# Kernel tuning notes

Hardware: AMD Instinct MI355X
Metric: run time of the kernel (lower is better)

Reference implementation:

```python
import jax, jax.numpy as jnp
import numpy as np

EPS = 1e-5  # matches torch default epsilon


def setup_inputs() -> dict:
    key = jax.random.key(0)
    ks = jax.random.split(key, 7)
    B, S, H = 32, 8192, 128
    return {
        "time_to_maturity": jax.random.uniform(ks[0], (B, S), jnp.float32),
        "log_moneyness": jax.random.normal(ks[1], (B, S), jnp.float32),
        "target_variance": jax.random.uniform(ks[2], (B, S), jnp.float32),
        "W1": jax.random.normal(ks[3], (2, H), jnp.float32) * 0.5,
        "b1": jax.random.normal(ks[4], (H,), jnp.float32) * 0.1,
        "W2": jax.random.normal(ks[5], (H,), jnp.float32) * 0.5,
        "b2": jax.random.normal(ks[6], (1,), jnp.float32) * 0.1,
    }


def reference(time_to_maturity, log_moneyness, target_variance, W1, b1, W2, b2):
    # Upstream surface model: elementwise (t, x) -> total implied variance w > 0.
    def w_fn(t, x):
        h = jnp.tanh(t * W1[0] + x * W1[1] + b1)  # [H]
        return jax.nn.softplus(jnp.dot(h, W2) + b2[0])  # scalar

    w_t_fn = jax.grad(w_fn, argnums=0)
    w_x_fn = jax.grad(w_fn, argnums=1)
    w_xx_fn = jax.grad(w_x_fn, argnums=1)

    tf = time_to_maturity.reshape(-1)   # [N] flattened query points
    xf = log_moneyness.reshape(-1)
    tgt = target_variance.reshape(-1)
    N = tf.shape[0]

    # Diagonal Jacobian entries: replaces the O(N^2) unit-vector autograd loop.
    w = jax.vmap(w_fn)(tf, xf)
    w_t = jax.vmap(w_t_fn)(tf, xf)
    w_x = jax.vmap(w_x_fn)(tf, xf)
    w_xx = jax.vmap(w_xx_fn)(tf, xf)

    percentage_error = (w - tgt) / (tgt + EPS)
    mspe = jnp.sum(percentage_error ** 2)

    calendar = jnp.sum(jnp.maximum(-w_t, 0.0) ** 2)

    # Durrleman butterfly condition g(x)
    g = (1.0 - xf * w_x / (2.0 * w)) ** 2 - (w_x / 4.0) * (1.0 / w + 0.25) + w_xx / 2.0
    butterfly = jnp.sum(jnp.maximum(-g, 0.0) ** 2)

    return jnp.stack([mspe, calendar, butterfly]) / N
```

## Files before the change

kernel.cpp:

```cpp
#include <hip/hip_runtime.h>
#include <cmath>

#define HDIM 128
constexpr float EPSF = 1e-5f;
constexpr float K2L  = 2.8853900817779268f;
constexpr float INVK = 0.34657359027997264f;
constexpr float L2E  = 1.4426950408889634f;
constexpr float LN2  = 0.6931471805599453f;

__device__ inline float fast_rcp(float x) { return __builtin_amdgcn_rcpf(x); }

__device__ inline float fast_exp2(float x) {
#if __has_builtin(__builtin_amdgcn_exp2f)
    return __builtin_amdgcn_exp2f(x);
#else
    float r; asm("v_exp_f32 %0, %1" : "=v"(r) : "v"(x)); return r;
#endif
}

__device__ inline float fast_log2(float x) {
#if __has_builtin(__builtin_amdgcn_logf)
    return __builtin_amdgcn_logf(x);
#else
    float r; asm("v_log_f32 %0, %1" : "=v"(r) : "v"(x)); return r;
#endif
}

__device__ inline double wave_reduce(double v) {
    #pragma unroll
    for (int off = 32; off > 0; off >>= 1)
        v += __shfl_down(v, off, 64);
    return v;
}

__global__ __launch_bounds__(256) void surf_loss_main(
    const float* __restrict__ tt, const float* __restrict__ xx,
    const float* __restrict__ tg,
    const float* __restrict__ W1, const float* __restrict__ b1,
    const float* __restrict__ W2, const float* __restrict__ b2,
    double* __restrict__ partials, int N)
{
    __shared__ float4 cs[HDIM];
    __shared__ float  cc[HDIM];
    __shared__ double sred[3][4];
    const int tid = threadIdx.x;
    for (int i = tid; i < HDIM; i += 256) {
        const float a = W1[i] * K2L;
        const float c = W1[HDIM + i] * K2L;
        const float b = b1[i] * K2L;
        cs[i] = make_float4(a, c, b, W2[i]);
        cc[i] = -2.f * c * c;
    }
    __syncthreads();
    const float b2v = b2[0];

    double mspe = 0.0, cal = 0.0, bfly = 0.0;
    for (int idx = blockIdx.x * 256 + tid; idx < N; idx += gridDim.x * 256) {
        const float t = tt[idx], x = xx[idx], tgt = tg[idx];
        float u = b2v, ut = 0.f, ux = 0.f, uxx = 0.f;
        #pragma unroll 8
        for (int i = 0; i < HDIM; ++i) {
            const float4 c = cs[i];
            const float zp = fmaf(t, c.x, fmaf(x, c.y, c.z));
            const float e  = fast_exp2(zp);
            const float r  = fast_rcp(e + 1.f);
            const float th = fmaf(-2.f, r, 1.f);
            const float d  = fmaf(-th, th, 1.f);
            const float wd = c.w * d;
            u   = fmaf(c.w, th, u);
            ut  = fmaf(wd, c.x, ut);
            ux  = fmaf(wd, c.y, ux);
            uxx = fmaf(wd * th, cc[i], uxx);
        }
        const float q  = fast_exp2(-fabsf(u) * L2E);
        const float rp = fast_rcp(1.f + q);
        const float s  = (u >= 0.f) ? rp : q * rp;
        const float w_log  = fmaxf(u, 0.f) + LN2 * fast_log2(1.f + q);
        const float w_tail = q * fmaf(-0.5f, q, 1.f);
        const float w  = (u < -9.f) ? w_tail : w_log;

        const float utt  = ut * INVK;
        const float uxt  = ux * INVK;
        const float uxxt = uxx * (INVK * INVK);
        const float w_t  = s * utt;
        const float w_x  = s * uxt;
        const float w_xx = fmaf(s * (1.f - s), uxt * uxt, s * uxxt);

        const float pe = (w - tgt) * fast_rcp(tgt + EPSF);
        mspe += (double)pe * (double)pe;

        const float ctm = fmaxf(-w_t, 0.f);
        cal += (double)ctm * (double)ctm;

        const float invw = fast_rcp(w);
        const float a1 = fmaf(-0.5f * x * w_x, invw, 1.f);
        const float g  = fmaf(0.5f, w_xx,
                         fmaf(a1, a1, -0.25f * w_x * (invw + 0.25f)));
        const float btm = fmaxf(-g, 0.f);
        bfly += (double)btm * (double)btm;
    }

    double v0 = wave_reduce(mspe), v1 = wave_reduce(cal), v2 = wave_reduce(bfly);
    const int wid = tid >> 6, lane = tid & 63;
    if (lane == 0) { sred[0][wid] = v0; sred[1][wid] = v1; sred[2][wid] = v2; }
    __syncthreads();
    if (tid == 0) {
        double a = 0, b = 0, c = 0;
        #pragma unroll
        for (int wv = 0; wv < 4; ++wv) { a += sred[0][wv]; b += sred[1][wv]; c += sred[2][wv]; }
        partials[blockIdx.x * 3 + 0] = a;
        partials[blockIdx.x * 3 + 1] = b;
        partials[blockIdx.x * 3 + 2] = c;
    }
}

__global__ __launch_bounds__(256) void surf_loss_final(
    const double* __restrict__ partials, int nblocks, float* __restrict__ out, int N)
{
    const int tid = threadIdx.x;
    double a = 0, b = 0, c = 0;
    for (int i = tid; i < nblocks; i += 256) {
        a += partials[i * 3 + 0];
        b += partials[i * 3 + 1];
        c += partials[i * 3 + 2];
    }
    a = wave_reduce(a); b = wave_reduce(b); c = wave_reduce(c);
    __shared__ double sred[3][4];
    const int wid = tid >> 6, lane = tid & 63;
    if (lane == 0) { sred[0][wid] = a; sred[1][wid] = b; sred[2][wid] = c; }
    __syncthreads();
    if (tid == 0) {
        const double inv = 1.0 / (double)N;
        double s0 = 0, s1 = 0, s2 = 0;
        #pragma unroll
        for (int wv = 0; wv < 4; ++wv) { s0 += sred[0][wv]; s1 += sred[1][wv]; s2 += sred[2][wv]; }
        out[0] = (float)(s0 * inv);
        out[1] = (float)(s1 * inv);
        out[2] = (float)(s2 * inv);
    }
}

extern "C" void kernel_launch(void* const* d_in, const int* in_sizes, int n_in,
                              void* d_out, int out_size, void* d_ws, size_t ws_size,
                              hipStream_t stream) {
    const float* tt = (const float*)d_in[0];
    const float* xx = (const float*)d_in[1];
    const float* tg = (const float*)d_in[2];
    const float* W1 = (const float*)d_in[3];
    const float* b1 = (const float*)d_in[4];
    const float* W2 = (const float*)d_in[5];
    const float* b2 = (const float*)d_in[6];
    const int N = in_sizes[0];

    int blocks = (N + 255) / 256;
    if (blocks > 1024) blocks = 1024;
    while ((size_t)blocks * 3 * sizeof(double) > ws_size && blocks > 1) blocks >>= 1;

    double* partials = (double*)d_ws;
    surf_loss_main<<<blocks, 256, 0, stream>>>(tt, xx, tg, W1, b1, W2, b2, partials, N);
    surf_loss_final<<<1, 256, 0, stream>>>(partials, blocks, (float*)d_out, N);
}
```

Measured before the change: 23.28 us.

## Vectorize hidden-unit loop with packed f32x2 FMAs and read weights directly

```diff
diff --git a/kernel.cpp b/kernel.cpp
--- a/kernel.cpp
+++ b/kernel.cpp
@@ -2,9 +2,10 @@
 #include <cmath>
 
 #define HDIM 128
+typedef float f32x2 __attribute__((ext_vector_type(2)));
+
 constexpr float EPSF = 1e-5f;
 constexpr float K2L  = 2.8853900817779268f;
-constexpr float INVK = 0.34657359027997264f;
 constexpr float L2E  = 1.4426950408889634f;
 constexpr float LN2  = 0.6931471805599453f;
 
@@ -26,6 +27,14 @@
 #endif
 }
 
+__device__ inline f32x2 pk_fma(f32x2 a, f32x2 b, f32x2 c) {
+#if __has_builtin(__builtin_elementwise_fma)
+    return __builtin_elementwise_fma(a, b, c);
+#else
+    f32x2 r; r.x = fmaf(a.x, b.x, c.x); r.y = fmaf(a.y, b.y, c.y); return r;
+#endif
+}
+
 __device__ inline double wave_reduce(double v) {
     #pragma unroll
     for (int off = 32; off > 0; off >>= 1)
@@ -33,71 +42,88 @@
     return v;
 }
 
-__global__ __launch_bounds__(256) void surf_loss_main(
+__device__ inline void point_epilogue(float u, float ut, float ux, float uxxp,
+                                      float x, float tgt,
+                                      double& mspe, double& cal, double& bfly)
+{
+    const float q  = fast_exp2(-fabsf(u) * L2E);
+    const float rp = fast_rcp(1.f + q);
+    const float s  = (u >= 0.f) ? rp : q * rp;
+    const float w_log  = fmaxf(u, 0.f) + LN2 * fast_log2(1.f + q);
+    const float w_tail = q * fmaf(-0.5f, q, 1.f);
+    const float w  = (u < -9.f) ? w_tail : w_log;
+
+    const float w_t  = s * ut;
+    const float w_x  = s * ux;
+    const float w_xx = fmaf(s * (1.f - s), ux * ux, -2.f * s * uxxp);
+
+    const float pe = (w - tgt) * fast_rcp(tgt + EPSF);
+    mspe += (double)pe * (double)pe;
+
+    const float ctm = fmaxf(-w_t, 0.f);
+    cal += (double)ctm * (double)ctm;
+
+    const float invw = fast_rcp(w);
+    const float a1 = fmaf(-0.5f * x * w_x, invw, 1.f);
+    const float g  = fmaf(0.5f, w_xx,
+                     fmaf(a1, a1, -0.25f * w_x * (invw + 0.25f)));
+    const float btm = fmaxf(-g, 0.f);
+    bfly += (double)btm * (double)btm;
+}
+
+__global__ __launch_bounds__(256, 4) void surf_loss_main(
     const float* __restrict__ tt, const float* __restrict__ xx,
     const float* __restrict__ tg,
     const float* __restrict__ W1, const float* __restrict__ b1,
     const float* __restrict__ W2, const float* __restrict__ b2,
     double* __restrict__ partials, int N)
 {
-    __shared__ float4 cs[HDIM];
-    __shared__ float  cc[HDIM];
     __shared__ double sred[3][4];
     const int tid = threadIdx.x;
-    for (int i = tid; i < HDIM; i += 256) {
-        const float a = W1[i] * K2L;
-        const float c = W1[HDIM + i] * K2L;
-        const float b = b1[i] * K2L;
-        cs[i] = make_float4(a, c, b, W2[i]);
-        cc[i] = -2.f * c * c;
-    }
-    __syncthreads();
+
+    const f32x2* __restrict__ A2 = (const f32x2*)(W1);
+    const f32x2* __restrict__ C2 = (const f32x2*)(W1 + HDIM);
+    const f32x2* __restrict__ B2 = (const f32x2*)(b1);
+    const f32x2* __restrict__ V2 = (const f32x2*)(W2);
     const float b2v = b2[0];
 
     double mspe = 0.0, cal = 0.0, bfly = 0.0;
+
     for (int idx = blockIdx.x * 256 + tid; idx < N; idx += gridDim.x * 256) {
         const float t = tt[idx], x = xx[idx], tgt = tg[idx];
-        float u = b2v, ut = 0.f, ux = 0.f, uxx = 0.f;
+        const f32x2 t2 = {t, t};
+        const f32x2 x2 = {x, x};
+        f32x2 u2   = {b2v, 0.f};
+        f32x2 ut2  = {0.f, 0.f};
+        f32x2 ux2  = {0.f, 0.f};
+        f32x2 uxx2 = {0.f, 0.f};
         #pragma unroll 8
-        for (int i = 0; i < HDIM; ++i) {
-            const float4 c = cs[i];
-            const float zp = fmaf(t, c.x, fmaf(x, c.y, c.z));
-            const float e  = fast_exp2(zp);
-            const float r  = fast_rcp(e + 1.f);
-            const float th = fmaf(-2.f, r, 1.f);
-            const float d  = fmaf(-th, th, 1.f);
-            const float wd = c.w * d;
-            u   = fmaf(c.w, th, u);
-            ut  = fmaf(wd, c.x, ut);
-            ux  = fmaf(wd, c.y, ux);
-            uxx = fmaf(wd * th, cc[i], uxx);
+        for (int i = 0; i < HDIM / 2; ++i) {
+            const f32x2 a = A2[i];
+            const f32x2 c = C2[i];
+            const f32x2 b = B2[i];
+            const f32x2 v = V2[i];
+            const f32x2 zc = x2 * c;
+            const f32x2 zb = zc + b;
+            const f32x2 z  = pk_fma(t2, a, zb);
+            const f32x2 zp = z * K2L;
+            f32x2 e;  e.x = fast_exp2(zp.x); e.y = fast_exp2(zp.y);
+            f32x2 r;  r.x = fast_rcp(e.x + 1.f); r.y = fast_rcp(e.y + 1.f);
+            const f32x2 th = pk_fma((f32x2){-2.f, -2.f}, r, (f32x2){1.f, 1.f});
+            const f32x2 d  = pk_fma(-th, th, (f32x2){1.f, 1.f});
+            const f32x2 wd = d * v;
+            u2   = pk_fma(th, v, u2);
+            ut2  = pk_fma(wd, a, ut2);
+            ux2  = pk_fma(wd, c, ux2);
+            const f32x2 wt  = wd * th;
+            const f32x2 wtc = wt * c;
+            uxx2 = pk_fma(wtc, c, uxx2);
         }
-        const float q  = fast_exp2(-fabsf(u) * L2E);
-        const float rp = fast_rcp(1.f + q);
-        const float s  = (u >= 0.f) ? rp : q * rp;
-        const float w_log  = fmaxf(u, 0.f) + LN2 * fast_log2(1.f + q);
-        const float w_tail = q * fmaf(-0.5f, q, 1.f);
-        const float w  = (u < -9.f) ? w_tail : w_log;
-
-        const float utt  = ut * INVK;
-        const float uxt  = ux * INVK;
-        const float uxxt = uxx * (INVK * INVK);
-        const float w_t  = s * utt;
-        const float w_x  = s * uxt;
-        const float w_xx = fmaf(s * (1.f - s), uxt * uxt, s * uxxt);
-
-        const float pe = (w - tgt) * fast_rcp(tgt + EPSF);
-        mspe += (double)pe * (double)pe;
-
-        const float ctm = fmaxf(-w_t, 0.f);
-        cal += (double)ctm * (double)ctm;
-
-        const float invw = fast_rcp(w);
-        const float a1 = fmaf(-0.5f * x * w_x, invw, 1.f);
-        const float g  = fmaf(0.5f, w_xx,
-                         fmaf(a1, a1, -0.25f * w_x * (invw + 0.25f)));
-        const float btm = fmaxf(-g, 0.f);
-        bfly += (double)btm * (double)btm;
+        const float u    = u2.x + u2.y;
+        const float ut   = ut2.x + ut2.y;
+        const float ux   = ux2.x + ux2.y;
+        const float uxxp = uxx2.x + uxx2.y;
+        point_epilogue(u, ut, ux, uxxp, x, tgt, mspe, cal, bfly);
     }
 
     double v0 = wave_reduce(mspe), v1 = wave_reduce(cal), v2 = wave_reduce(bfly);
```

After: 21.86 us. 1.07x faster.
